# Optimization experiments

Hardware: AMD Instinct MI355X
Metric: run time of the kernel (lower is better)

Reference implementation:

```python
import jax, jax.numpy as jnp
import numpy as np

N_HEAD = 8
LN_EPS = 1e-5


def _head_causal_conv(x, w, bias):
    # x: (b,T,N,d) -> per-head causal conv over T with kernel (1,3), pad-left 2
    b, T, N, d = x.shape
    dph = d // N_HEAD
    xh = x.reshape(b, T, N, N_HEAD, dph).transpose(0, 3, 4, 2, 1)  # (b,h,dph,N,T)
    xh = xh.reshape(b * N_HEAD, dph, N, T)
    y = jax.lax.conv_general_dilated(
        xh, w, window_strides=(1, 1), padding=[(0, 0), (2, 0)],
        dimension_numbers=("NCHW", "OIHW", "NCHW"))
    y = y + bias[None, :, None, None]
    C = w.shape[0]
    return y.reshape(b, N_HEAD, C, N, T).transpose(1, 0, 4, 3, 2)  # (h,b,T,N,C)


def setup_inputs() -> dict:
    key = jax.random.key(0)
    ks = jax.random.split(key, 12)
    b, T, N, d, C = 16, 36, 207, 64, 64
    dph = d // N_HEAD
    f32 = jnp.float32
    return {
        "X": jax.random.normal(ks[0], (b, T, N, d), f32),
        "Q": jax.random.normal(ks[1], (b, T, N, d), f32),
        "K": jax.random.normal(ks[2], (b, T, N, d), f32),
        "V": jax.random.normal(ks[3], (b, T, N, d), f32),
        "Wv": jax.random.normal(ks[4], (d, d), f32) * 0.05,
        "bv": jax.random.normal(ks[5], (d,), f32) * 0.05,
        "Wo": jax.random.normal(ks[6], (d, d), f32) * 0.05,
        "bo": jax.random.normal(ks[7], (d,), f32) * 0.05,
        "conv_q_w": jax.random.normal(ks[8], (C, dph, 1, 3), f32) * 0.05,
        "conv_q_b": jax.random.normal(ks[9], (C,), f32) * 0.05,
        "conv_k_w": jax.random.normal(ks[10], (C, dph, 1, 3), f32) * 0.05,
        "conv_k_b": jax.random.normal(ks[11], (C,), f32) * 0.05,
        "ln_gamma": jnp.ones((d,), f32),
        "ln_beta": jnp.zeros((d,), f32),
    }


def reference(X, Q, K, V, Wv, bv, Wo, bo, conv_q_w, conv_q_b, conv_k_w, conv_k_b, ln_gamma, ln_beta):
    b, T, N, d = V.shape
    dph = d // N_HEAD
    # value projection, split heads -> (h,b,T,N,dph)
    Vh = (V @ Wv.T + bv).reshape(b, T, N, N_HEAD, dph).transpose(3, 0, 1, 2, 4)
    # causal-conv Q/K generation per head -> (h,b,T,N,C)
    Qh = _head_causal_conv(Q, conv_q_w, conv_q_b)
    Kh = _head_causal_conv(K, conv_k_w, conv_k_b)
    C = Qh.shape[-1]
    scale = 1.0 / jnp.sqrt(jnp.asarray(C, Qh.dtype))
    # temporal attention per node: (h,b,N,Tq,Tk)
    scores = jnp.einsum("hbqnc,hbknc->hbnqk", Qh, Kh) * scale
    causal = jnp.tril(jnp.ones((T, T), bool))
    scores = jnp.where(causal, scores, jnp.finfo(scores.dtype).min)
    attn = jax.nn.softmax(scores, axis=-1)
    ctx = jnp.einsum("hbnqk,hbkne->hbqne", attn, Vh)  # (h,b,T,N,dph)
    out = ctx.transpose(1, 2, 3, 0, 4).reshape(b, T, N, d)
    out = out @ Wo.T + bo + X  # output proj + residual
    mu = out.mean(-1, keepdims=True)
    var = out.var(-1, keepdims=True)
    return (out - mu) / jnp.sqrt(var + LN_EPS) * ln_gamma + ln_beta
```

## Files before the change

kernel.cpp:

```cpp
#include <hip/hip_runtime.h>
#include <hip/hip_bf16.h>

#define TT 36
#define NN 207
#define LN_EPS 1e-5f

typedef __attribute__((ext_vector_type(8))) short short8;
typedef __attribute__((ext_vector_type(4))) float f32x4;

__device__ __forceinline__ unsigned short f2b(float f) {
    union { __hip_bfloat16 h; unsigned short u; } x;
    x.h = __float2bfloat16(f);
    return x.u;
}
__device__ __forceinline__ short8 s8(uint4 u) { union { uint4 a; short8 b; } x; x.a = u; return x.b; }

__global__ __launch_bounds__(512) void prep_kernel(
    const float* __restrict__ Wv, const float* __restrict__ Wo,
    const float* __restrict__ cqw, const float* __restrict__ cqb,
    const float* __restrict__ ckw, unsigned short* __restrict__ ws)
{
    const int tid = threadIdx.x;
    for (int i = tid; i < 4096; i += 512) {
        ws[1024 + i] = f2b(Wv[i]);
        ws[5120 + i] = f2b(Wo[i]);
    }
    for (int u = tid; u < 1024; u += 512) {
        int j2 = u >> 5, jp = u & 31;
        float acc = 0.f;
        if (j2 < 24 && jp < 25) {
            int wkc = (j2 & 7) * 3 + (j2 >> 3);
            if (jp < 24) {
                int wqc = (jp & 7) * 3 + (jp >> 3);
                for (int c = 0; c < 64; ++c) acc += cqw[c * 24 + wqc] * ckw[c * 24 + wkc];
            } else {
                for (int c = 0; c < 64; ++c) acc += cqb[c] * ckw[c * 24 + wkc];
            }
            acc *= 0.125f;
        }
        ws[u] = f2b(acc);
    }
}

__global__ __launch_bounds__(512, 4) void fused_attn12(
    const float* __restrict__ X, const float* __restrict__ Qg,
    const float* __restrict__ Kg, const float* __restrict__ Vg,
    const float* __restrict__ bv, const float* __restrict__ bo,
    const float* __restrict__ gam, const float* __restrict__ bet,
    const unsigned short* __restrict__ ws,
    float* __restrict__ out)
{
    __shared__ __align__(16) unsigned short Qs[40 * 72];
    __shared__ __align__(16) unsigned short Ks[40 * 72];
    __shared__ __align__(16) unsigned short VhT[64 * 40];
    __shared__ __align__(16) unsigned char  Pbuf[23040];

    unsigned short* Vs    = (unsigned short*)Pbuf;
    float*          OutS  = (float*)Pbuf;
    unsigned short* Ctx16 = Qs;

    const unsigned short* MtG = ws;
    const unsigned short* WvG = ws + 1024;
    const unsigned short* WoG = ws + 5120;

    const int tid  = threadIdx.x;
    const int lane = tid & 63;
    const int wave = tid >> 6;
    const int g    = lane >> 4, c15 = lane & 15;
    const int b    = blockIdx.x / NN;
    const int n    = blockIdx.x % NN;
    const uint4 z4 = {0u, 0u, 0u, 0u};

    const float4* Q4 = (const float4*)(Qg + (size_t)(b * TT * NN + n) * 64);
    const float4* K4 = (const float4*)(Kg + (size_t)(b * TT * NN + n) * 64);
    const float4* V4 = (const float4*)(Vg + (size_t)(b * TT * NN + n) * 64);
    for (int idx = tid; idx < TT * 16; idx += 512) {
        int t = idx >> 4, o = idx & 15;
        float4 q = Q4[t * 3312 + o];
        float4 k = K4[t * 3312 + o];
        float4 v = V4[t * 3312 + o];
        ushort4 qp = {f2b(q.x), f2b(q.y), f2b(q.z), f2b(q.w)};
        ushort4 kp = {f2b(k.x), f2b(k.y), f2b(k.z), f2b(k.w)};
        ushort4 vp = {f2b(v.x), f2b(v.y), f2b(v.z), f2b(v.w)};
        *(ushort4*)&Qs[t * 72 + o * 4] = qp;
        *(ushort4*)&Ks[t * 72 + o * 4] = kp;
        *(ushort4*)&Vs[t * 72 + o * 4] = vp;
    }
    for (int idx = tid; idx < 72; idx += 512) {
        if (idx < 36) ((uint4*)&Qs[36 * 72])[idx] = z4;
        else          ((uint4*)&Ks[36 * 72])[idx - 36] = z4;
    }
    if (tid < 64) *(uint2*)&VhT[tid * 40 + 36] = make_uint2(0u, 0u);
    __syncthreads();

    {
        #pragma unroll
        for (int tt = 0; tt < 2; ++tt) {
            int rt, ct;
            if (wave < 4) { rt = tt * 2; ct = wave; }
            else { if (tt) break; rt = 1; ct = wave - 4; }
            float bvv = bv[ct * 16 + c15];
            f32x4 d = {bvv, bvv, bvv, bvv};
            int rc = min(rt * 16 + c15, 35);
            uint4 A0 = *(const uint4*)&Vs[rc * 72 + g * 8];
            uint4 A1 = *(const uint4*)&Vs[rc * 72 + 32 + g * 8];
            uint4 B0 = *(const uint4*)&WvG[(ct * 16 + c15) * 64 + g * 8];
            uint4 B1 = *(const uint4*)&WvG[(ct * 16 + c15) * 64 + 32 + g * 8];
            d = __builtin_amdgcn_mfma_f32_16x16x32_bf16(s8(A0), s8(B0), d, 0, 0, 0);
            d = __builtin_amdgcn_mfma_f32_16x16x32_bf16(s8(A1), s8(B1), d, 0, 0, 0);
            int ts = rt * 16 + g * 4;
            if (ts < 36) {
                ushort4 o4 = {f2b(d[0]), f2b(d[1]), f2b(d[2]), f2b(d[3])};
                *(ushort4*)&VhT[(ct * 16 + c15) * 40 + ts] = o4;
            }
        }
    }
    __syncthreads();

    const int h8 = wave * 8;
    unsigned short* Ph = (unsigned short*)Pbuf + wave * 1440;
    {
        uint4 Af[2];
        #pragma unroll
        for (int mt = 0; mt < 2; ++mt)
            Af[mt] = *(const uint4*)&MtG[(mt * 16 + c15) * 32 + g * 8];
        #pragma unroll
        for (int qt = 0; qt < 3; ++qt) {
            uint4 bq;
            if (g == 3) { bq = z4; bq.x = 0x00003F80u; }
            else {
                int row = qt * 16 + c15 + g - 2;
                int rcq = min(max(row, 0), 39);
                bq = *(const uint4*)&Qs[rcq * 72 + h8];
                if (row < 0) bq = z4;
            }
            const int q = qt * 16 + c15;
            #pragma unroll
            for (int mt = 0; mt < 2; ++mt) {
                f32x4 zero = {0.f, 0.f, 0.f, 0.f};
                f32x4 d = __builtin_amdgcn_mfma_f32_16x16x32_bf16(s8(Af[mt]), s8(bq), zero, 0, 0, 0);
                if (q < 36) {
                    ushort4 o4 = {f2b(d[0]), f2b(d[1]), f2b(d[2]), f2b(d[3])};
                    *(ushort4*)&Ph[q * 40 + mt * 16 + g * 4] = o4;
                }
            }
        }
    }
    __syncthreads();

    {
        uint4 Ak[3], Zq[3];
        #pragma unroll
        for (int kt = 0; kt < 3; ++kt) {
            uint4 v = z4;
            if (g < 3) {
                int row = kt * 16 + c15 + g - 2;
                int rck = min(max(row, 0), 39);
                v = *(const uint4*)&Ks[rck * 72 + h8];
                if (row < 0) v = z4;
            }
            Ak[kt] = v;
        }
        #pragma unroll
        for (int qt = 0; qt < 3; ++qt) {
            int rcq = min(qt * 16 + c15, 35);
            Zq[qt] = *(const uint4*)&Ph[rcq * 40 + g * 8];
        }
        #pragma unroll
        for (int qt = 0; qt < 3; ++qt) {
            const int q = qt * 16 + c15;
            const bool qok = (qt < 2) || (c15 < 4);
            #pragma unroll
            for (int kt = 0; kt < 3; ++kt) {
                const int k0 = kt * 16 + g * 4;
                const bool can = qok && ((kt < 2) || (g < 2));
                if (kt <= qt) {
                    f32x4 zero = {0.f, 0.f, 0.f, 0.f};
                    f32x4 s = __builtin_amdgcn_mfma_f32_16x16x32_bf16(s8(Ak[kt]), s8(Zq[qt]), zero, 0, 0, 0);
                    if (can) {
                        ushort4 o4;
                        if (kt == qt) {
                            o4.x = (k0 + 0 <= q) ? f2b(__expf(s[0])) : (unsigned short)0;
                            o4.y = (k0 + 1 <= q) ? f2b(__expf(s[1])) : (unsigned short)0;
                            o4.z = (k0 + 2 <= q) ? f2b(__expf(s[2])) : (unsigned short)0;
                            o4.w = (k0 + 3 <= q) ? f2b(__expf(s[3])) : (unsigned short)0;
                        } else {
                            o4.x = f2b(__expf(s[0])); o4.y = f2b(__expf(s[1]));
                            o4.z = f2b(__expf(s[2])); o4.w = f2b(__expf(s[3]));
                        }
                        *(ushort4*)&Ph[q * 40 + k0] = o4;
                    }
                } else {
                    if (can) {
                        ushort4 zz = {0, 0, 0, 0};
                        *(ushort4*)&Ph[q * 40 + k0] = zz;
                    }
                }
            }
        }
    }

    {
        const unsigned ONE2 = 0x3F803F80u;
        uint4 A0, A1;
        if (c15 == 8) {
            A0 = make_uint4(ONE2, ONE2, ONE2, ONE2);
            A1 = (g == 0) ? make_uint4(ONE2, ONE2, 0u, 0u) : z4;
        } else if (c15 < 8) {
            A0 = *(const uint4*)&VhT[(h8 + c15) * 40 + g * 8];
            A1 = (g == 0) ? *(const uint4*)&VhT[(h8 + c15) * 40 + 32] : z4;
        } else { A0 = z4; A1 = z4; }
        #pragma unroll
        for (int qt = 0; qt < 3; ++qt) {
            int rcq = min(qt * 16 + c15, 35);
            uint4 B0 = *(const uint4*)&Ph[rcq * 40 + g * 8];
            uint4 B1 = (g == 0) ? *(const uint4*)&Ph[rcq * 40 + 32] : z4;
            f32x4 d = {0.f, 0.f, 0.f, 0.f};
            d = __builtin_amdgcn_mfma_f32_16x16x32_bf16(s8(A0), s8(B0), d, 0, 0, 0);
            d = __builtin_amdgcn_mfma_f32_16x16x32_bf16(s8(A1), s8(B1), d, 0, 0, 0);
            float es = __shfl(d[0], 32 + c15);
            float rcp = __frcp_rn(es);
            const int q = qt * 16 + c15;
            if (g < 2 && ((qt < 2) || (c15 < 4))) {
                ushort4 o4 = {f2b(d[0] * rcp), f2b(d[1] * rcp), f2b(d[2] * rcp), f2b(d[3] * rcp)};
                *(ushort4*)&Ctx16[q * 72 + h8 + g * 4] = o4;
            }
        }
    }
    __syncthreads();

    {
        const int ot = (wave < 4) ? wave : wave - 4;
        uint4 A0 = *(const uint4*)&WoG[(ot * 16 + c15) * 64 + g * 8];
        uint4 A1 = *(const uint4*)&WoG[(ot * 16 + c15) * 64 + 32 + g * 8];
        float4 bo4 = ((const float4*)bo)[ot * 4 + g];
        #pragma unroll
        for (int pass = 0; pass < 2; ++pass) {
            int nt;
            if (wave < 4) nt = pass * 2;
            else { if (pass) break; nt = 1; }
            int rct = min(nt * 16 + c15, 35);
            uint4 B0 = *(const uint4*)&Ctx16[rct * 72 + g * 8];
            uint4 B1 = *(const uint4*)&Ctx16[rct * 72 + 32 + g * 8];
            f32x4 d = {bo4.x, bo4.y, bo4.z, bo4.w};
            d = __builtin_amdgcn_mfma_f32_16x16x32_bf16(s8(A0), s8(B0), d, 0, 0, 0);
            d = __builtin_amdgcn_mfma_f32_16x16x32_bf16(s8(A1), s8(B1), d, 0, 0, 0);
            const int t = nt * 16 + c15;
            const int o0 = ot * 16 + g * 4;
            if (t < 36) {
                size_t gi = ((size_t)(b * TT + t) * NN + n) * 64 + o0;
                float4 xv = *(const float4*)&X[gi];
                float4 ov = {d[0] + xv.x, d[1] + xv.y, d[2] + xv.z, d[3] + xv.w};
                *(float4*)&OutS[t * 68 + o0] = ov;
            }
        }
    }
    __syncthreads();

    {
        float gamr = gam[lane], betr = bet[lane];
        for (int t = wave; t < TT; t += 8) {
            float acc = OutS[t * 68 + lane];
            float s1 = acc, s2 = acc * acc;
            #pragma unroll
            for (int off = 32; off; off >>= 1) {
                s1 += __shfl_xor(s1, off);
                s2 += __shfl_xor(s2, off);
            }
            float mu  = s1 * (1.f / 64.f);
            float var = s2 * (1.f / 64.f) - mu * mu;
            size_t gi = ((size_t)(b * TT + t) * NN + n) * 64 + lane;
            out[gi] = (acc - mu) * rsqrtf(var + LN_EPS) * gamr + betr;
        }
    }
}

extern "C" void kernel_launch(void* const* d_in, const int* in_sizes, int n_in,
                              void* d_out, int out_size, void* d_ws, size_t ws_size,
                              hipStream_t stream) {
    const float* X   = (const float*)d_in[0];
    const float* Q   = (const float*)d_in[1];
    const float* K   = (const float*)d_in[2];
    const float* V   = (const float*)d_in[3];
    const float* Wv  = (const float*)d_in[4];
    const float* bv  = (const float*)d_in[5];
    const float* Wo  = (const float*)d_in[6];
    const float* bo  = (const float*)d_in[7];
    const float* cqw = (const float*)d_in[8];
    const float* cqb = (const float*)d_in[9];
    const float* ckw = (const float*)d_in[10];
    const float* gam = (const float*)d_in[12];
    const float* bet = (const float*)d_in[13];
    float* out = (float*)d_out;
    unsigned short* ws = (unsigned short*)d_ws;

    hipLaunchKernelGGL(prep_kernel, dim3(1), dim3(512), 0, stream, Wv, Wo, cqw, cqb, ckw, ws);
    hipLaunchKernelGGL(fused_attn12, dim3(16 * NN), dim3(512), 0, stream,
                       X, Q, K, V, bv, bo, gam, bet, ws, out);
}
```

Baseline: 79.25 us.

## Load V straight into MFMA registers and prefetch X, Wo, and biases early

The V tile no longer goes through shared memory: each lane reads its fp32 V row slice from global memory, packs it to bf16 in registers and feeds it to the value-projection MFMA. This removes a shared-memory staging pass and the barrier that followed it. The X residual, Wo fragments, biases and LayerNorm parameters are now loaded at kernel start so their latency overlaps the Q/K staging. The Q/K shared buffers shrink and their padding rows are no longer zeroed. Holding the prefetched values raises register pressure, and the V reads are less coalesced.

```diff
diff --git a/kernel.cpp b/kernel.cpp
--- a/kernel.cpp
+++ b/kernel.cpp
@@ -14,6 +14,12 @@
     return x.u;
 }
 __device__ __forceinline__ short8 s8(uint4 u) { union { uint4 a; short8 b; } x; x.a = u; return x.b; }
+__device__ __forceinline__ uint4 pack8(float4 a, float4 b) {
+    union { struct { ushort4 l, h; } s; uint4 u; } x;
+    x.s.l = make_ushort4(f2b(a.x), f2b(a.y), f2b(a.z), f2b(a.w));
+    x.s.h = make_ushort4(f2b(b.x), f2b(b.y), f2b(b.z), f2b(b.w));
+    return x.u;
+}
 
 __global__ __launch_bounds__(512) void prep_kernel(
     const float* __restrict__ Wv, const float* __restrict__ Wo,
@@ -42,7 +48,7 @@
     }
 }
 
-__global__ __launch_bounds__(512, 4) void fused_attn12(
+__global__ __launch_bounds__(512, 4) void fused_attn15(
     const float* __restrict__ X, const float* __restrict__ Qg,
     const float* __restrict__ Kg, const float* __restrict__ Vg,
     const float* __restrict__ bv, const float* __restrict__ bo,
@@ -50,12 +56,11 @@
     const unsigned short* __restrict__ ws,
     float* __restrict__ out)
 {
-    __shared__ __align__(16) unsigned short Qs[40 * 72];
-    __shared__ __align__(16) unsigned short Ks[40 * 72];
+    __shared__ __align__(16) unsigned short Qs[36 * 72];
+    __shared__ __align__(16) unsigned short Ks[36 * 72];
     __shared__ __align__(16) unsigned short VhT[64 * 40];
     __shared__ __align__(16) unsigned char  Pbuf[23040];
 
-    unsigned short* Vs    = (unsigned short*)Pbuf;
     float*          OutS  = (float*)Pbuf;
     unsigned short* Ctx16 = Qs;
 
@@ -71,47 +76,58 @@
     const int n    = blockIdx.x % NN;
     const uint4 z4 = {0u, 0u, 0u, 0u};
 
+    const int ot = (wave < 4) ? wave : wave - 4;
+    uint4 WoA0 = *(const uint4*)&WoG[(ot * 16 + c15) * 64 + g * 8];
+    uint4 WoA1 = *(const uint4*)&WoG[(ot * 16 + c15) * 64 + 32 + g * 8];
+    float4 bo4 = ((const float4*)bo)[ot * 4 + g];
+    float  bvv = bv[ot * 16 + c15];
+    float  gamr = gam[lane], betr = bet[lane];
+    const int nt0 = (wave < 4) ? 0 : 1;
+    const int t0  = nt0 * 16 + c15;
+    const size_t Xbase0 = ((size_t)(b * TT + min(t0, 35)) * NN + n) * 64 + ot * 16 + g * 4;
+    float4 xv0 = *(const float4*)&X[Xbase0];
+    float4 xv1 = {0.f, 0.f, 0.f, 0.f};
+    if (wave < 4) {
+        const int t1 = 32 + c15;
+        xv1 = *(const float4*)&X[((size_t)(b * TT + min(t1, 35)) * NN + n) * 64 + ot * 16 + g * 4];
+    }
+
     const float4* Q4 = (const float4*)(Qg + (size_t)(b * TT * NN + n) * 64);
     const float4* K4 = (const float4*)(Kg + (size_t)(b * TT * NN + n) * 64);
-    const float4* V4 = (const float4*)(Vg + (size_t)(b * TT * NN + n) * 64);
     for (int idx = tid; idx < TT * 16; idx += 512) {
         int t = idx >> 4, o = idx & 15;
         float4 q = Q4[t * 3312 + o];
         float4 k = K4[t * 3312 + o];
-        float4 v = V4[t * 3312 + o];
         ushort4 qp = {f2b(q.x), f2b(q.y), f2b(q.z), f2b(q.w)};
         ushort4 kp = {f2b(k.x), f2b(k.y), f2b(k.z), f2b(k.w)};
-        ushort4 vp = {f2b(v.x), f2b(v.y), f2b(v.z), f2b(v.w)};
         *(ushort4*)&Qs[t * 72 + o * 4] = qp;
         *(ushort4*)&Ks[t * 72 + o * 4] = kp;
-        *(ushort4*)&Vs[t * 72 + o * 4] = vp;
-    }
-    for (int idx = tid; idx < 72; idx += 512) {
-        if (idx < 36) ((uint4*)&Qs[36 * 72])[idx] = z4;
-        else          ((uint4*)&Ks[36 * 72])[idx - 36] = z4;
     }
     if (tid < 64) *(uint2*)&VhT[tid * 40 + 36] = make_uint2(0u, 0u);
-    __syncthreads();
-
-    {
+
+    {
+        uint4 B0 = *(const uint4*)&WvG[(ot * 16 + c15) * 64 + g * 8];
+        uint4 B1 = *(const uint4*)&WvG[(ot * 16 + c15) * 64 + 32 + g * 8];
         #pragma unroll
         for (int tt = 0; tt < 2; ++tt) {
-            int rt, ct;
-            if (wave < 4) { rt = tt * 2; ct = wave; }
-            else { if (tt) break; rt = 1; ct = wave - 4; }
-            float bvv = bv[ct * 16 + c15];
+            int rt;
+            if (wave < 4) rt = tt * 2;
+            else { if (tt) break; rt = 1; }
+            int rc = min(rt * 16 + c15, 35);
+            const float* vrow = Vg + ((size_t)(b * TT + rc) * NN + n) * 64;
+            float4 va = *(const float4*)(vrow + g * 8);
+            float4 vb = *(const float4*)(vrow + g * 8 + 4);
+            float4 vc = *(const float4*)(vrow + 32 + g * 8);
+            float4 vd = *(const float4*)(vrow + 32 + g * 8 + 4);
+            uint4 A0 = pack8(va, vb);
+            uint4 A1 = pack8(vc, vd);
             f32x4 d = {bvv, bvv, bvv, bvv};
-            int rc = min(rt * 16 + c15, 35);
-            uint4 A0 = *(const uint4*)&Vs[rc * 72 + g * 8];
-            uint4 A1 = *(const uint4*)&Vs[rc * 72 + 32 + g * 8];
-            uint4 B0 = *(const uint4*)&WvG[(ct * 16 + c15) * 64 + g * 8];
-            uint4 B1 = *(const uint4*)&WvG[(ct * 16 + c15) * 64 + 32 + g * 8];
             d = __builtin_amdgcn_mfma_f32_16x16x32_bf16(s8(A0), s8(B0), d, 0, 0, 0);
             d = __builtin_amdgcn_mfma_f32_16x16x32_bf16(s8(A1), s8(B1), d, 0, 0, 0);
             int ts = rt * 16 + g * 4;
             if (ts < 36) {
                 ushort4 o4 = {f2b(d[0]), f2b(d[1]), f2b(d[2]), f2b(d[3])};
-                *(ushort4*)&VhT[(ct * 16 + c15) * 40 + ts] = o4;
+                *(ushort4*)&VhT[(ot * 16 + c15) * 40 + ts] = o4;
             }
         }
     }
@@ -130,7 +146,7 @@
             if (g == 3) { bq = z4; bq.x = 0x00003F80u; }
             else {
                 int row = qt * 16 + c15 + g - 2;
-                int rcq = min(max(row, 0), 39);
+                int rcq = min(max(row, 0), 35);
                 bq = *(const uint4*)&Qs[rcq * 72 + h8];
                 if (row < 0) bq = z4;
             }
@@ -155,7 +171,7 @@
             uint4 v = z4;
             if (g < 3) {
                 int row = kt * 16 + c15 + g - 2;
-                int rck = min(max(row, 0), 39);
+                int rck = min(max(row, 0), 35);
                 v = *(const uint4*)&Ks[rck * 72 + h8];
                 if (row < 0) v = z4;
             }
@@ -230,26 +246,21 @@
     __syncthreads();
 
     {
-        const int ot = (wave < 4) ? wave : wave - 4;
-        uint4 A0 = *(const uint4*)&WoG[(ot * 16 + c15) * 64 + g * 8];
-        uint4 A1 = *(const uint4*)&WoG[(ot * 16 + c15) * 64 + 32 + g * 8];
-        float4 bo4 = ((const float4*)bo)[ot * 4 + g];
         #pragma unroll
         for (int pass = 0; pass < 2; ++pass) {
             int nt;
-            if (wave < 4) nt = pass * 2;
-            else { if (pass) break; nt = 1; }
+            float4 xv;
+            if (wave < 4) { nt = pass * 2; xv = pass ? xv1 : xv0; }
+            else { if (pass) break; nt = 1; xv = xv0; }
             int rct = min(nt * 16 + c15, 35);
             uint4 B0 = *(const uint4*)&Ctx16[rct * 72 + g * 8];
             uint4 B1 = *(const uint4*)&Ctx16[rct * 72 + 32 + g * 8];
             f32x4 d = {bo4.x, bo4.y, bo4.z, bo4.w};
-            d = __builtin_amdgcn_mfma_f32_16x16x32_bf16(s8(A0), s8(B0), d, 0, 0, 0);
-            d = __builtin_amdgcn_mfma_f32_16x16x32_bf16(s8(A1), s8(B1), d, 0, 0, 0);
+            d = __builtin_amdgcn_mfma_f32_16x16x32_bf16(s8(WoA0), s8(B0), d, 0, 0, 0);
+            d = __builtin_amdgcn_mfma_f32_16x16x32_bf16(s8(WoA1), s8(B1), d, 0, 0, 0);
             const int t = nt * 16 + c15;
             const int o0 = ot * 16 + g * 4;
             if (t < 36) {
-                size_t gi = ((size_t)(b * TT + t) * NN + n) * 64 + o0;
-                float4 xv = *(const float4*)&X[gi];
                 float4 ov = {d[0] + xv.x, d[1] + xv.y, d[2] + xv.z, d[3] + xv.w};
                 *(float4*)&OutS[t * 68 + o0] = ov;
             }
@@ -258,7 +269,6 @@
     __syncthreads();
 
     {
-        float gamr = gam[lane], betr = bet[lane];
         for (int t = wave; t < TT; t += 8) {
             float acc = OutS[t * 68 + lane];
             float s1 = acc, s2 = acc * acc;
@@ -295,6 +305,6 @@
     unsigned short* ws = (unsigned short*)d_ws;
 
     hipLaunchKernelGGL(prep_kernel, dim3(1), dim3(512), 0, stream, Wv, Wo, cqw, cqb, ckw, ws);
-    hipLaunchKernelGGL(fused_attn12, dim3(16 * NN), dim3(512), 0, stream,
+    hipLaunchKernelGGL(fused_attn15, dim3(16 * NN), dim3(512), 0, stream,
                        X, Q, K, V, bv, bo, gam, bet, ws, out);
 }
```

Measured after the change: 90.85 us. +14.6%, slower.
